# Kernel optimization log

Hardware: AMD Instinct MI355X
Metric: run time of the kernel (lower is better)

## Reference

```python
import jax, jax.numpy as jnp
import numpy as np

B, T, C, H, R = 2, 2048, 2048, 16, 8
D = C // H  # head_dim = 128


def _rope_cache(seq_len, dim, theta=10000.0):
    pos = jnp.arange(seq_len, dtype=jnp.float32)[:, None]            # [T,1]
    idx = jnp.arange(0, dim, 2, dtype=jnp.float32)                   # [D/2]
    freqs = 1.0 / (theta ** (idx / dim))
    ang = pos * freqs                                                # [T, D/2]
    return jnp.cos(ang), jnp.sin(ang)


def setup_inputs() -> dict:
    key = jax.random.key(0)
    ks = jax.random.split(key, 16)
    s = 0.02
    inp = {"x": jax.random.normal(ks[0], (B, T, C), dtype=jnp.float32)}
    i = 1
    for nm in ("q", "k", "v", "p"):
        inp[f"{nm}_w"] = jax.random.normal(ks[i], (C, C), dtype=jnp.float32) * s; i += 1
        inp[f"{nm}_b"] = jnp.zeros((C,), dtype=jnp.float32)
        inp[f"{nm}_A"] = jax.random.normal(ks[i], (C, R), dtype=jnp.float32) * s; i += 1
        inp[f"{nm}_B"] = jax.random.normal(ks[i], (R, C), dtype=jnp.float32) * s; i += 1
    cos, sin = _rope_cache(T, D)
    inp["cos"] = cos
    inp["sin"] = sin
    inp["mask"] = jnp.tril(jnp.ones((T, T), dtype=bool))  # causal SDPA mask
    inp["use_lora"] = 1
    return inp


def _lora_linear(x, w, b, A, Bm, use_lora):
    # base GEMM + bias, plus low-rank adapter x @ A @ B (intended path)
    out = x @ w.T + b
    if use_lora:
        out = out + (x @ A) @ Bm
    return out


def _apply_rope(x, cos, sin):
    # x: [B,H,T,D]; cos/sin: [T, D/2] broadcast over batch & heads
    x1 = x[..., ::2]
    x2 = x[..., 1::2]
    y = jnp.stack((x1 * cos - x2 * sin, x1 * sin + x2 * cos), axis=-1)
    return y.reshape(x.shape)


def reference(x, q_w, q_b, q_A, q_B, k_w, k_b, k_A, k_B,
              v_w, v_b, v_A, v_B, p_w, p_b, p_A, p_B,
              cos, sin, mask, use_lora):
    Bsz, Tl, Cd = x.shape
    q = _lora_linear(x, q_w, q_b, q_A, q_B, use_lora).reshape(Bsz, Tl, H, D).transpose(0, 2, 1, 3)
    k = _lora_linear(x, k_w, k_b, k_A, k_B, use_lora).reshape(Bsz, Tl, H, D).transpose(0, 2, 1, 3)
    v = _lora_linear(x, v_w, v_b, v_A, v_B, use_lora).reshape(Bsz, Tl, H, D).transpose(0, 2, 1, 3)
    q = _apply_rope(q, cos, sin)
    k = _apply_rope(k, cos, sin)
    # scaled dot-product attention with boolean mask (True = attend)
    scale = 1.0 / jnp.sqrt(jnp.asarray(D, dtype=x.dtype))
    scores = jnp.einsum('bhqd,bhkd->bhqk', q, k) * scale          # [B,H,T,T]
    neg = jnp.asarray(jnp.finfo(scores.dtype).min, dtype=scores.dtype)
    scores = jnp.where(mask, scores, neg)
    attn = jax.nn.softmax(scores, axis=-1)
    out = jnp.einsum('bhqk,bhkd->bhqd', attn, v)                  # [B,H,T,D]
    y = out.transpose(0, 2, 1, 3).reshape(Bsz, Tl, Cd)
    return _lora_linear(y, p_w, p_b, p_A, p_B, use_lora)
```

## Files before the change

### kernel.cpp

```cpp
#include <hip/hip_runtime.h>

typedef _Float16 f16;
typedef _Float16 f16x4 __attribute__((ext_vector_type(4)));
typedef _Float16 f16x8 __attribute__((ext_vector_type(8)));
typedef __fp16 hf2 __attribute__((ext_vector_type(2)));
typedef float f32x4 __attribute__((ext_vector_type(4)));

#define DEV static __device__ __forceinline__

DEV void gl_lds16(const void* g, void* l) {
  __builtin_amdgcn_global_load_lds(
      (const __attribute__((address_space(1))) void*)g,
      (__attribute__((address_space(3))) void*)l, 16, 0, 0);
}

DEV uint pkrtz(float a, float b) {
  hf2 h = __builtin_amdgcn_cvt_pkrtz(a, b);
  return __builtin_bit_cast(uint, h);
}

DEV f32x4 MFMA(f16x8 a, f16x8 b, f32x4 c) {
  return __builtin_amdgcn_mfma_f32_16x16x32_f16(a, b, c, 0, 0, 0);
}

#define SC2Q 0.12752551286084103f

__global__ void cast_w_kernel(const float* __restrict__ w0,
                              const float* __restrict__ w1,
                              const float* __restrict__ w2,
                              const float* __restrict__ w3,
                              f16* __restrict__ b0, f16* __restrict__ b1,
                              f16* __restrict__ b2, f16* __restrict__ b3) {
  const int total4 = 4 * 4194304 / 4;
  for (int i = blockIdx.x * blockDim.x + threadIdx.x; i < total4;
       i += gridDim.x * blockDim.x) {
    int e = i << 2;
    const float* s; f16* d; int off;
    if (e < 4194304)        { s = w0; d = b0; off = e; }
    else if (e < 8388608)   { s = w1; d = b1; off = e - 4194304; }
    else if (e < 12582912)  { s = w2; d = b2; off = e - 8388608; }
    else                    { s = w3; d = b3; off = e - 12582912; }
    float4 v = *(const float4*)(s + off);
    f16x4 hv = {(f16)v.x, (f16)v.y, (f16)v.z, (f16)v.w};
    *(f16x4*)(d + off) = hv;
  }
}

__global__ __launch_bounds__(256) void lora_x_kernel(
    const float* __restrict__ x, const float* __restrict__ Aq,
    const float* __restrict__ Ak, const float* __restrict__ Av,
    float* __restrict__ la, f16* __restrict__ xb) {
  const int wave = threadIdx.x >> 6, lane = threadIdx.x & 63;
  const int m = blockIdx.x * 4 + wave;
  const float* xrow = x + (size_t)m * 2048;
  f16* xbrow = xb + (size_t)m * 2048;
  const float* As[3] = {Aq, Ak, Av};
  float acc[3][8] = {};
  for (int i = 0; i < 32; ++i) {
    int k = i * 64 + lane;
    float xv = xrow[k];
    xbrow[k] = (f16)xv;
#pragma unroll
    for (int nm = 0; nm < 3; ++nm) {
      const float4* ap = (const float4*)(As[nm] + (size_t)k * 8);
      float4 a0 = ap[0], a1 = ap[1];
      acc[nm][0] += xv * a0.x; acc[nm][1] += xv * a0.y;
      acc[nm][2] += xv * a0.z; acc[nm][3] += xv * a0.w;
      acc[nm][4] += xv * a1.x; acc[nm][5] += xv * a1.y;
      acc[nm][6] += xv * a1.z; acc[nm][7] += xv * a1.w;
    }
  }
#pragma unroll
  for (int nm = 0; nm < 3; ++nm)
#pragma unroll
    for (int r = 0; r < 8; ++r) {
      float v = acc[nm][r];
#pragma unroll
      for (int off = 1; off < 64; off <<= 1) v += __shfl_xor(v, off);
      acc[nm][r] = v;
    }
  if (lane == 0) {
#pragma unroll
    for (int nm = 0; nm < 3; ++nm)
#pragma unroll
      for (int r = 0; r < 8; ++r)
        la[nm * 32768 + (size_t)m * 8 + r] = acc[nm][r];
  }
}

__global__ __launch_bounds__(256) void lora_p_kernel(
    const f16* __restrict__ y, const float* __restrict__ Ap,
    float* __restrict__ lap) {
  const int wave = threadIdx.x >> 6, lane = threadIdx.x & 63;
  const int m = blockIdx.x * 4 + wave;
  const f16* yrow = y + (size_t)m * 2048;
  float acc[8] = {};
  for (int i = 0; i < 4; ++i) {
    int k0 = i * 512 + lane * 8;
    f16x8 yv = *(const f16x8*)(yrow + k0);
#pragma unroll
    for (int j = 0; j < 8; ++j) {
      float xv = (float)yv[j];
      const float4* ap = (const float4*)(Ap + (size_t)(k0 + j) * 8);
      float4 a0 = ap[0], a1 = ap[1];
      acc[0] += xv * a0.x; acc[1] += xv * a0.y;
      acc[2] += xv * a0.z; acc[3] += xv * a0.w;
      acc[4] += xv * a1.x; acc[5] += xv * a1.y;
      acc[6] += xv * a1.z; acc[7] += xv * a1.w;
    }
  }
#pragma unroll
  for (int r = 0; r < 8; ++r) {
    float v = acc[r];
#pragma unroll
    for (int off = 1; off < 64; off <<= 1) v += __shfl_xor(v, off);
    acc[r] = v;
  }
  if (lane == 0) {
#pragma unroll
    for (int r = 0; r < 8; ++r) lap[(size_t)m * 8 + r] = acc[r];
  }
}

struct GemmArgs {
  const f16* A;
  const f16* W[3];
  const float* bias[3];
  const float* la[3];
  const float* Bm[3];
  void* out[3];
  int mode[3];
};

__global__ __launch_bounds__(256, 2) void gemm2_kernel(
    GemmArgs args, const int* __restrict__ use_lora,
    const float* __restrict__ cosT, const float* __restrict__ sinT) {
  extern __shared__ char smem[];
  const int z = blockIdx.y;
  const f16* A = args.A;
  const f16* Bw = args.W[z];
  const float* bias = args.bias[z];
  const float* la = args.la[z];
  const float* Bm = args.Bm[z];
  void* out = args.out[z];
  const int mode = args.mode[z];

  const int tid = threadIdx.x;
  const int wave = tid >> 6, lane = tid & 63;
  const int lr = lane & 15, lg = lane >> 4;
  const int bm = (int)blockIdx.x >> 4, bn = (int)blockIdx.x & 15;
  const int m0 = bm << 7, n0 = bn << 7;
  const int wr = wave >> 1, wc = wave & 1;

  const char* Ab = (const char*)A;
  const char* Bb = (const char*)Bw;

  uint aoff[4], boff[4];
#pragma unroll
  for (int r = 0; r < 4; ++r) {
    uint beta = (uint)(wave * 4 + r) * 1024 + (uint)lane * 16;
    uint row = beta >> 7;
    uint c = (beta & 127u) ^ ((row & 7u) << 4);
    aoff[r] = (uint)(m0 + row) * 4096 + c;
    boff[r] = (uint)(n0 + row) * 4096 + c;
  }

  auto STAGE = [&](int kt, int b) {
    char* dst = smem + b * 32768;
    const size_t kb = (size_t)kt << 7;
#pragma unroll
    for (int r = 0; r < 4; ++r) {
      gl_lds16(Ab + (aoff[r] + kb), dst + (wave * 4 + r) * 1024);
      gl_lds16(Bb + (boff[r] + kb), dst + 16384 + (wave * 4 + r) * 1024);
    }
  };

  f32x4 acc[4][4] = {};

  STAGE(0, 0);
  for (int kt = 0; kt < 32; ++kt) {
    const int b = kt & 1;
    asm volatile("s_waitcnt vmcnt(0) lgkmcnt(0)" ::: "memory");
    __builtin_amdgcn_s_barrier();
    if (kt + 1 < 32) STAGE(kt + 1, b ^ 1);

    const char* buf = smem + b * 32768;
    f16x8 af[2][4], bf[2][4];
#pragma unroll
    for (int ks = 0; ks < 2; ++ks) {
#pragma unroll
      for (int mi = 0; mi < 4; ++mi) {
        int row = wr * 64 + mi * 16 + lr;
        int c = (ks * 64 + lg * 16) ^ ((row & 7) << 4);
        af[ks][mi] = *(const f16x8*)(buf + row * 128 + c);
      }
#pragma unroll
      for (int ni = 0; ni < 4; ++ni) {
        int row = wc * 64 + ni * 16 + lr;
        int c = (ks * 64 + lg * 16) ^ ((row & 7) << 4);
        bf[ks][ni] = *(const f16x8*)(buf + 16384 + row * 128 + c);
      }
    }
    __builtin_amdgcn_s_setprio(1);
#pragma unroll
    for (int ks = 0; ks < 2; ++ks)
#pragma unroll
      for (int mi = 0; mi < 4; ++mi)
#pragma unroll
        for (int ni = 0; ni < 4; ++ni)
          acc[mi][ni] = MFMA(af[ks][mi], bf[ks][ni], acc[mi][ni]);
    __builtin_amdgcn_s_setprio(0);
  }

  const int ul = use_lora[0];
  asm volatile("s_waitcnt lgkmcnt(0)" ::: "memory");
  __builtin_amdgcn_s_barrier();

  float bv[4], bml[4][8];
#pragma unroll
  for (int ni = 0; ni < 4; ++ni) {
    int n = n0 + wc * 64 + ni * 16 + lr;
    bv[ni] = bias[n];
    if (ul) {
#pragma unroll
      for (int r = 0; r < 8; ++r) bml[ni][r] = Bm[r * 2048 + n];
    }
  }

#pragma unroll
  for (int mi = 0; mi < 4; ++mi) {
    const int mbase = m0 + wr * 64 + mi * 16 + lg * 4;
    float lar[4][8];
    if (ul) {
#pragma unroll
      for (int rg = 0; rg < 4; ++rg) {
        const float4* lp = (const float4*)(la + (size_t)(mbase + rg) * 8);
        float4 l0 = lp[0], l1 = lp[1];
        lar[rg][0] = l0.x; lar[rg][1] = l0.y; lar[rg][2] = l0.z; lar[rg][3] = l0.w;
        lar[rg][4] = l1.x; lar[rg][5] = l1.y; lar[rg][6] = l1.z; lar[rg][7] = l1.w;
      }
    }
#pragma unroll
    for (int ni = 0; ni < 4; ++ni) {
      const int n = n0 + wc * 64 + ni * 16 + lr;
#pragma unroll
      for (int rg = 0; rg < 4; ++rg) {
        float v = acc[mi][ni][rg] + bv[ni];
        if (ul) {
#pragma unroll
          for (int r = 0; r < 8; ++r) v += lar[rg][r] * bml[ni][r];
        }
        const int mm = wr * 64 + mi * 16 + lg * 4 + rg;
        const int nn = wc * 64 + ni * 16 + lr;
        if (mode <= 1) {
          float pv = __shfl_xor(v, 1);
          const int t = (mbase + rg) & 2047;
          const int ci = t * 64 + ((n & 127) >> 1);
          float cs = cosT[ci], sn = sinT[ci];
          float res = ((lane & 1) == 0) ? (v * cs - pv * sn)
                                        : (pv * sn + v * cs);
          if (mode == 0) res *= SC2Q;
          ((f16*)smem)[mm * 128 + nn] = (f16)res;
        } else if (mode == 2) {
          *(f16*)(smem + nn * 256 + ((mm * 2) ^ ((nn & 7) << 4))) = (f16)v;
        } else {
          ((float*)out)[(size_t)(mbase + rg) * 2048 + n] = v;
        }
      }
    }
  }

  if (mode <= 1) {
    __builtin_amdgcn_s_barrier();
    const long b_ = m0 >> 11;
    const int tb = m0 & 2047;
    char* obase = (char*)out + ((b_ * 16 + bn) * 2048 + tb) * 256;
#pragma unroll
    for (int p = 0; p < 8; ++p) {
      int s = p * 4096 + tid * 16;
      int row = s >> 8, c = s & 255;
      *(uint4*)(obase + (long)row * 256 + c) = *(const uint4*)(smem + s);
    }
  } else if (mode == 2) {
    __builtin_amdgcn_s_barrier();
    const long b_ = m0 >> 11;
    const int tb = m0 & 2047;
    char* obase = (char*)out + (((b_ * 16 + bn) * 128) * 2048 + tb) * 2;
#pragma unroll
    for (int p = 0; p < 8; ++p) {
      int s = p * 4096 + tid * 16;
      int row = s >> 8, cb = s & 255;
      int c = cb ^ ((row & 7) << 4);
      uint4 val = *(const uint4*)(smem + row * 256 + c);
      *(uint4*)(obase + (long)row * 4096 + cb) = val;
    }
  }
}

__global__ __launch_bounds__(256, 2) void attn_kernel(
    const f16* __restrict__ qr, const f16* __restrict__ kr,
    const f16* __restrict__ vt, f16* __restrict__ y) {
  extern __shared__ char smem[];
  const int tid = threadIdx.x, wave = tid >> 6, lane = tid & 63;
  const int lr = lane & 15, lg = lane >> 4;
  const int qt = 15 - (int)blockIdx.x;
  const int q0 = qt << 7;
  const int h = blockIdx.y, b = blockIdx.z;
  const long bh = b * 16 + h;
  const int nt = 2 * qt + 2;

  const char* kbase = (const char*)kr + bh * 2048 * 256;
  const char* vbase = (const char*)vt + bh * 128 * 4096;

  uint koff[4], voff[4];
#pragma unroll
  for (int r = 0; r < 4; ++r) {
    uint s = (uint)(wave * 4 + r) * 1024 + (uint)lane * 16;
    uint rowk = s >> 8;
    koff[r] = rowk * 256 + ((s & 255u) ^ ((rowk & 7u) << 4));
    uint rowv = s >> 7;
    voff[r] = rowv * 4096 + ((s & 127u) ^ ((rowv & 7u) << 4));
  }

  f16x8 qf[2][4];
#pragma unroll
  for (int g = 0; g < 2; ++g) {
    const char* qb =
        (const char*)qr + (bh * 2048 + q0 + wave * 32 + g * 16 + lr) * 256;
#pragma unroll
    for (int ks = 0; ks < 4; ++ks)
      qf[g][ks] = *(const f16x8*)(qb + ks * 64 + lg * 16);
  }

  f32x4 o[2][8] = {};
  float mrow[2] = {-3e38f, -3e38f};
  float lsum[2] = {0.f, 0.f};

  auto STAGE = [&](int kv0, int bsel) {
    char* Ks = smem + bsel * 32768;
    char* Vs = Ks + 16384;
#pragma unroll
    for (int r = 0; r < 4; ++r) {
      gl_lds16(kbase + (size_t)kv0 * 256 + koff[r], Ks + (wave * 4 + r) * 1024);
      gl_lds16(vbase + (size_t)kv0 * 2 + voff[r], Vs + (wave * 4 + r) * 1024);
    }
  };

  STAGE(0, 0);
  __syncthreads();

  for (int kt = 0; kt < nt; ++kt) {
    const int kv0 = kt << 6;
    if (kt + 1 < nt) STAGE((kt + 1) << 6, (kt + 1) & 1);
    const char* Ks = smem + (kt & 1) * 32768;
    const char* Vs = Ks + 16384;

    if (kv0 <= q0 + wave * 32 + 31) {
      f32x4 sa[2][4] = {};
      __builtin_amdgcn_s_setprio(1);
#pragma unroll
      for (int ks = 0; ks < 4; ++ks)
#pragma unroll
        for (int n = 0; n < 4; ++n) {
          int row = n * 16 + lr;
          int c = (ks * 64 + lg * 16) ^ ((row & 7) << 4);
          f16x8 kf = *(const f16x8*)(Ks + row * 256 + c);
          sa[0][n] = MFMA(kf, qf[0][ks], sa[0][n]);
          sa[1][n] = MFMA(kf, qf[1][ks], sa[1][n]);
        }
      __builtin_amdgcn_s_setprio(0);

      f16x8 pf[2][2];
#pragma unroll
      for (int g = 0; g < 2; ++g) {
        const int qgbase = q0 + wave * 32 + g * 16;
        float L[16];
        const bool dm = (kv0 + 63 > qgbase);
#pragma unroll
        for (int n = 0; n < 4; ++n)
#pragma unroll
          for (int rg = 0; rg < 4; ++rg) {
            float Lv = sa[g][n][rg];
            if (dm && (kv0 + n * 16 + lg * 4 + rg > qgbase + lr)) Lv = -3e37f;
            L[n * 4 + rg] = Lv;
          }
        float m0a = fmaxf(L[0], L[1]),  m1a = fmaxf(L[2], L[3]);
        float m2a = fmaxf(L[4], L[5]),  m3a = fmaxf(L[6], L[7]);
        float m4a = fmaxf(L[8], L[9]),  m5a = fmaxf(L[10], L[11]);
        float m6a = fmaxf(L[12], L[13]), m7a = fmaxf(L[14], L[15]);
        float m0b = fmaxf(m0a, m1a), m1b = fmaxf(m2a, m3a);
        float m2b = fmaxf(m4a, m5a), m3b = fmaxf(m6a, m7a);
        float pm = fmaxf(fmaxf(m0b, m1b), fmaxf(m2b, m3b));
        if (!__all(pm <= mrow[g] + 8.f)) {
          pm = fmaxf(pm, __shfl_xor(pm, 16));
          pm = fmaxf(pm, __shfl_xor(pm, 32));
          float mn = fmaxf(mrow[g], pm);
          float alpha = exp2f(mrow[g] - mn);
          mrow[g] = mn;
          lsum[g] *= alpha;
#pragma unroll
          for (int dt = 0; dt < 8; ++dt)
#pragma unroll
            for (int rg = 0; rg < 4; ++rg) o[g][dt][rg] *= alpha;
        }
        const float mn = mrow[g];
#pragma unroll
        for (int i = 0; i < 16; ++i) L[i] = exp2f(L[i] - mn);
        float s0 = L[0] + L[1], s1 = L[2] + L[3], s2 = L[4] + L[5],
              s3 = L[6] + L[7], s4 = L[8] + L[9], s5 = L[10] + L[11],
              s6 = L[12] + L[13], s7 = L[14] + L[15];
        float t0 = s0 + s1, t1 = s2 + s3, t2 = s4 + s5, t3 = s6 + s7;
        float ps = (t0 + t1) + (t2 + t3);
        ps += __shfl_xor(ps, 16);
        ps += __shfl_xor(ps, 32);
        lsum[g] += ps;

#pragma unroll
        for (int ks2 = 0; ks2 < 2; ++ks2) {
          uint w0 = pkrtz(L[8 * ks2 + 0], L[8 * ks2 + 1]);
          uint w1 = pkrtz(L[8 * ks2 + 2], L[8 * ks2 + 3]);
          uint w2 = pkrtz(L[8 * ks2 + 4], L[8 * ks2 + 5]);
          uint w3 = pkrtz(L[8 * ks2 + 6], L[8 * ks2 + 7]);
          int src1 = ((lg & 1) << 5) + lr;
          int src2 = src1 + 16;
          uint a0 = __shfl((int)w0, src1), a1 = __shfl((int)w1, src1);
          uint a2 = __shfl((int)w2, src1), a3 = __shfl((int)w3, src1);
          uint b0 = __shfl((int)w0, src2), b1 = __shfl((int)w1, src2);
          uint b2 = __shfl((int)w2, src2), b3 = __shfl((int)w3, src2);
          const bool hi = (lg >> 1) != 0;
          uint4 uu;
          uu.x = hi ? a2 : a0;
          uu.y = hi ? a3 : a1;
          uu.z = hi ? b2 : b0;
          uu.w = hi ? b3 : b1;
          pf[g][ks2] = __builtin_bit_cast(f16x8, uu);
        }
      }

#pragma unroll
      for (int ks2 = 0; ks2 < 2; ++ks2) {
        __builtin_amdgcn_s_setprio(1);
#pragma unroll
        for (int dt = 0; dt < 8; ++dt) {
          int drow = dt * 16 + lr;
          int c = (ks2 * 64 + lg * 16) ^ ((drow & 7) << 4);
          f16x8 vf = *(const f16x8*)(Vs + drow * 128 + c);
          o[0][dt] = MFMA(vf, pf[0][ks2], o[0][dt]);
          o[1][dt] = MFMA(vf, pf[1][ks2], o[1][dt]);
        }
        __builtin_amdgcn_s_setprio(0);
      }
    }
    __syncthreads();
  }

#pragma unroll
  for (int g = 0; g < 2; ++g) {
    const float inv = 1.f / lsum[g];
    const int row = wave * 32 + g * 16 + lr;
#pragma unroll
    for (int dt = 0; dt < 8; ++dt) {
      uint lo = pkrtz(o[g][dt][0] * inv, o[g][dt][1] * inv);
      uint hi2 = pkrtz(o[g][dt][2] * inv, o[g][dt][3] * inv);
      int c = (dt * 32 + lg * 8) ^ ((row & 7) << 4);
      uint2 w;
      w.x = lo;
      w.y = hi2;
      *(uint2*)(smem + row * 256 + c) = w;
    }
  }
  __syncthreads();
#pragma unroll
  for (int p = 0; p < 8; ++p) {
    int s = p * 4096 + tid * 16;
    int row = s >> 8, cb = s & 255;
    int c = cb ^ ((row & 7) << 4);
    char* dst =
        (char*)y + ((long)(b * 2048 + q0 + row) * 2048 + h * 128) * 2 + cb;
    *(uint4*)dst = *(const uint4*)(smem + row * 256 + c);
  }
}

extern "C" void kernel_launch(void* const* d_in, const int* in_sizes, int n_in,
                              void* d_out, int out_size, void* d_ws,
                              size_t ws_size, hipStream_t stream) {
  (void)in_sizes; (void)n_in; (void)out_size; (void)ws_size;
  const float* x   = (const float*)d_in[0];
  const float* q_w = (const float*)d_in[1];
  const float* q_b = (const float*)d_in[2];
  const float* q_A = (const float*)d_in[3];
  const float* q_B = (const float*)d_in[4];
  const float* k_w = (const float*)d_in[5];
  const float* k_b = (const float*)d_in[6];
  const float* k_A = (const float*)d_in[7];
  const float* k_B = (const float*)d_in[8];
  const float* v_w = (const float*)d_in[9];
  const float* v_b = (const float*)d_in[10];
  const float* v_A = (const float*)d_in[11];
  const float* v_B = (const float*)d_in[12];
  const float* p_w = (const float*)d_in[13];
  const float* p_b = (const float*)d_in[14];
  const float* p_A = (const float*)d_in[15];
  const float* p_B = (const float*)d_in[16];
  const float* cosT = (const float*)d_in[17];
  const float* sinT = (const float*)d_in[18];
  const int* use_lora = (const int*)d_in[20];

  char* ws = (char*)d_ws;
  f16* xb  = (f16*)(ws);
  f16* wqb = (f16*)(ws + 16777216);
  f16* wkb = (f16*)(ws + 25165824);
  f16* wvb = (f16*)(ws + 33554432);
  f16* wpb = (f16*)(ws + 41943040);
  float* la = (float*)(ws + 50331648);
  f16* qr  = (f16*)(ws + 50855936);
  f16* kr  = (f16*)(ws + 67633152);
  f16* vt  = (f16*)(ws + 84410368);
  f16* y   = xb;
  float* lap = la + 98304;

  cast_w_kernel<<<dim3(2048), dim3(256), 0, stream>>>(
      q_w, k_w, v_w, p_w, wqb, wkb, wvb, wpb);
  lora_x_kernel<<<dim3(1024), dim3(256), 0, stream>>>(x, q_A, k_A, v_A, la, xb);

  GemmArgs qkv;
  qkv.A = xb;
  qkv.W[0] = wqb;  qkv.W[1] = wkb;  qkv.W[2] = wvb;
  qkv.bias[0] = q_b; qkv.bias[1] = k_b; qkv.bias[2] = v_b;
  qkv.la[0] = la; qkv.la[1] = la + 32768; qkv.la[2] = la + 65536;
  qkv.Bm[0] = q_B; qkv.Bm[1] = k_B; qkv.Bm[2] = v_B;
  qkv.out[0] = qr; qkv.out[1] = kr; qkv.out[2] = vt;
  qkv.mode[0] = 0; qkv.mode[1] = 1; qkv.mode[2] = 2;
  gemm2_kernel<<<dim3(512, 3), dim3(256), 65536, stream>>>(
      qkv, use_lora, cosT, sinT);

  attn_kernel<<<dim3(16, 16, 2), dim3(256), 65536, stream>>>(qr, kr, vt, y);
  lora_p_kernel<<<dim3(1024), dim3(256), 0, stream>>>(y, p_A, lap);

  GemmArgs pp;
  pp.A = y;
  pp.W[0] = wpb;  pp.W[1] = wpb;  pp.W[2] = wpb;
  pp.bias[0] = p_b; pp.bias[1] = p_b; pp.bias[2] = p_b;
  pp.la[0] = lap; pp.la[1] = lap; pp.la[2] = lap;
  pp.Bm[0] = p_B; pp.Bm[1] = p_B; pp.Bm[2] = p_B;
  pp.out[0] = d_out; pp.out[1] = d_out; pp.out[2] = d_out;
  pp.mode[0] = 3; pp.mode[1] = 3; pp.mode[2] = 3;
  gemm2_kernel<<<dim3(512, 1), dim3(256), 65536, stream>>>(
      pp, use_lora, nullptr, nullptr);
}
```

Measured before the change: 369.6 us.

## Software-pipeline attention: overlap next tile's QK^T with current softmax and PV

```diff
diff --git a/kernel.cpp b/kernel.cpp
--- a/kernel.cpp
+++ b/kernel.cpp
@@ -308,6 +308,7 @@
   const int h = blockIdx.y, b = blockIdx.z;
   const long bh = b * 16 + h;
   const int nt = 2 * qt + 2;
+  const int wbound = q0 + wave * 32 + 31;
 
   const char* kbase = (const char*)kr + bh * 2048 * 256;
   const char* vbase = (const char*)vt + bh * 128 * 4096;
@@ -336,122 +337,141 @@
   float mrow[2] = {-3e38f, -3e38f};
   float lsum[2] = {0.f, 0.f};
 
-  auto STAGE = [&](int kv0, int bsel) {
-    char* Ks = smem + bsel * 32768;
-    char* Vs = Ks + 16384;
-#pragma unroll
-    for (int r = 0; r < 4; ++r) {
+  auto STAGE_K = [&](int kv0, int kbi) {
+    char* Ks = smem + kbi * 16384;
+#pragma unroll
+    for (int r = 0; r < 4; ++r)
       gl_lds16(kbase + (size_t)kv0 * 256 + koff[r], Ks + (wave * 4 + r) * 1024);
+  };
+  auto STAGE_V = [&](int kv0, int vbi) {
+    char* Vs = smem + 49152 + vbi * 16384;
+#pragma unroll
+    for (int r = 0; r < 4; ++r)
       gl_lds16(vbase + (size_t)kv0 * 2 + voff[r], Vs + (wave * 4 + r) * 1024);
-    }
   };
 
-  STAGE(0, 0);
+  auto QKT = [&](int kbi, f32x4 (&sa)[2][4]) {
+    const char* Ks = smem + kbi * 16384;
+#pragma unroll
+    for (int g = 0; g < 2; ++g)
+#pragma unroll
+      for (int n = 0; n < 4; ++n) sa[g][n] = f32x4{0.f, 0.f, 0.f, 0.f};
+    __builtin_amdgcn_s_setprio(1);
+#pragma unroll
+    for (int ks = 0; ks < 4; ++ks)
+#pragma unroll
+      for (int n = 0; n < 4; ++n) {
+        int row = n * 16 + lr;
+        int c = (ks * 64 + lg * 16) ^ ((row & 7) << 4);
+        f16x8 kf = *(const f16x8*)(Ks + row * 256 + c);
+        sa[0][n] = MFMA(kf, qf[0][ks], sa[0][n]);
+        sa[1][n] = MFMA(kf, qf[1][ks], sa[1][n]);
+      }
+    __builtin_amdgcn_s_setprio(0);
+  };
+
+  auto SOFTMAX_PV = [&](int kt, f32x4 (&sa)[2][4]) {
+    const int kv0 = kt << 6;
+    const char* Vs = smem + 49152 + (kt & 1) * 16384;
+    f16x8 pf[2][2];
+#pragma unroll
+    for (int g = 0; g < 2; ++g) {
+      const int qgbase = q0 + wave * 32 + g * 16;
+      float L[16];
+      const bool dm = (kv0 + 63 > qgbase);
+#pragma unroll
+      for (int n = 0; n < 4; ++n)
+#pragma unroll
+        for (int rg = 0; rg < 4; ++rg) {
+          float Lv = sa[g][n][rg];
+          if (dm && (kv0 + n * 16 + lg * 4 + rg > qgbase + lr)) Lv = -3e37f;
+          L[n * 4 + rg] = Lv;
+        }
+      float m0a = fmaxf(L[0], L[1]),  m1a = fmaxf(L[2], L[3]);
+      float m2a = fmaxf(L[4], L[5]),  m3a = fmaxf(L[6], L[7]);
+      float m4a = fmaxf(L[8], L[9]),  m5a = fmaxf(L[10], L[11]);
+      float m6a = fmaxf(L[12], L[13]), m7a = fmaxf(L[14], L[15]);
+      float m0b = fmaxf(m0a, m1a), m1b = fmaxf(m2a, m3a);
+      float m2b = fmaxf(m4a, m5a), m3b = fmaxf(m6a, m7a);
+      float pm = fmaxf(fmaxf(m0b, m1b), fmaxf(m2b, m3b));
+      if (!__all(pm <= mrow[g] + 8.f)) {
+        pm = fmaxf(pm, __shfl_xor(pm, 16));
+        pm = fmaxf(pm, __shfl_xor(pm, 32));
+        float mn = fmaxf(mrow[g], pm);
+        float alpha = exp2f(mrow[g] - mn);
+        mrow[g] = mn;
+        lsum[g] *= alpha;
+#pragma unroll
+        for (int dt = 0; dt < 8; ++dt)
+#pragma unroll
+          for (int rg = 0; rg < 4; ++rg) o[g][dt][rg] *= alpha;
+      }
+      const float mn = mrow[g];
+#pragma unroll
+      for (int i = 0; i < 16; ++i) L[i] = exp2f(L[i] - mn);
+      float s0 = L[0] + L[1], s1 = L[2] + L[3], s2 = L[4] + L[5],
+            s3 = L[6] + L[7], s4 = L[8] + L[9], s5 = L[10] + L[11],
+            s6 = L[12] + L[13], s7 = L[14] + L[15];
+      float t0 = s0 + s1, t1 = s2 + s3, t2 = s4 + s5, t3 = s6 + s7;
+      float ps = (t0 + t1) + (t2 + t3);
+      ps += __shfl_xor(ps, 16);
+      ps += __shfl_xor(ps, 32);
+      lsum[g] += ps;
+
+#pragma unroll
+      for (int ks2 = 0; ks2 < 2; ++ks2) {
+        uint w0 = pkrtz(L[8 * ks2 + 0], L[8 * ks2 + 1]);
+        uint w1 = pkrtz(L[8 * ks2 + 2], L[8 * ks2 + 3]);
+        uint w2 = pkrtz(L[8 * ks2 + 4], L[8 * ks2 + 5]);
+        uint w3 = pkrtz(L[8 * ks2 + 6], L[8 * ks2 + 7]);
+        int src1 = ((lg & 1) << 5) + lr;
+        int src2 = src1 + 16;
+        uint a0 = __shfl((int)w0, src1), a1 = __shfl((int)w1, src1);
+        uint a2 = __shfl((int)w2, src1), a3 = __shfl((int)w3, src1);
+        uint b0 = __shfl((int)w0, src2), b1 = __shfl((int)w1, src2);
+        uint b2 = __shfl((int)w2, src2), b3 = __shfl((int)w3, src2);
+        const bool hi = (lg >> 1) != 0;
+        uint4 uu;
+        uu.x = hi ? a2 : a0;
+        uu.y = hi ? a3 : a1;
+        uu.z = hi ? b2 : b0;
+        uu.w = hi ? b3 : b1;
+        pf[g][ks2] = __builtin_bit_cast(f16x8, uu);
+      }
+    }
+#pragma unroll
+    for (int ks2 = 0; ks2 < 2; ++ks2) {
+      __builtin_amdgcn_s_setprio(1);
+#pragma unroll
+      for (int dt = 0; dt < 8; ++dt) {
+        int drow = dt * 16 + lr;
+        int c = (ks2 * 64 + lg * 16) ^ ((drow & 7) << 4);
+        f16x8 vf = *(const f16x8*)(Vs + drow * 128 + c);
+        o[0][dt] = MFMA(vf, pf[0][ks2], o[0][dt]);
+        o[1][dt] = MFMA(vf, pf[1][ks2], o[1][dt]);
+      }
+      __builtin_amdgcn_s_setprio(0);
+    }
+  };
+
+  auto ITER = [&](int kt, f32x4 (&cur)[2][4], f32x4 (&nxt)[2][4]) {
+    if (kt + 1 < nt) STAGE_V((kt + 1) << 6, (kt + 1) & 1);
+    if (kt + 2 < nt) STAGE_K((kt + 2) << 6, (kt + 2) % 3);
+    if (kt + 1 < nt && ((kt + 1) << 6) <= wbound) QKT((kt + 1) % 3, nxt);
+    if ((kt << 6) <= wbound) SOFTMAX_PV(kt, cur);
+    __syncthreads();
+  };
+
+  STAGE_K(0, 0);
+  STAGE_V(0, 0);
+  STAGE_K(64, 1);
   __syncthreads();
-
-  for (int kt = 0; kt < nt; ++kt) {
-    const int kv0 = kt << 6;
-    if (kt + 1 < nt) STAGE((kt + 1) << 6, (kt + 1) & 1);
-    const char* Ks = smem + (kt & 1) * 32768;
-    const char* Vs = Ks + 16384;
-
-    if (kv0 <= q0 + wave * 32 + 31) {
-      f32x4 sa[2][4] = {};
-      __builtin_amdgcn_s_setprio(1);
-#pragma unroll
-      for (int ks = 0; ks < 4; ++ks)
-#pragma unroll
-        for (int n = 0; n < 4; ++n) {
-          int row = n * 16 + lr;
-          int c = (ks * 64 + lg * 16) ^ ((row & 7) << 4);
-          f16x8 kf = *(const f16x8*)(Ks + row * 256 + c);
-          sa[0][n] = MFMA(kf, qf[0][ks], sa[0][n]);
-          sa[1][n] = MFMA(kf, qf[1][ks], sa[1][n]);
-        }
-      __builtin_amdgcn_s_setprio(0);
-
-      f16x8 pf[2][2];
-#pragma unroll
-      for (int g = 0; g < 2; ++g) {
-        const int qgbase = q0 + wave * 32 + g * 16;
-        float L[16];
-        const bool dm = (kv0 + 63 > qgbase);
-#pragma unroll
-        for (int n = 0; n < 4; ++n)
-#pragma unroll
-          for (int rg = 0; rg < 4; ++rg) {
-            float Lv = sa[g][n][rg];
-            if (dm && (kv0 + n * 16 + lg * 4 + rg > qgbase + lr)) Lv = -3e37f;
-            L[n * 4 + rg] = Lv;
-          }
-        float m0a = fmaxf(L[0], L[1]),  m1a = fmaxf(L[2], L[3]);
-        float m2a = fmaxf(L[4], L[5]),  m3a = fmaxf(L[6], L[7]);
-        float m4a = fmaxf(L[8], L[9]),  m5a = fmaxf(L[10], L[11]);
-        float m6a = fmaxf(L[12], L[13]), m7a = fmaxf(L[14], L[15]);
-        float m0b = fmaxf(m0a, m1a), m1b = fmaxf(m2a, m3a);
-        float m2b = fmaxf(m4a, m5a), m3b = fmaxf(m6a, m7a);
-        float pm = fmaxf(fmaxf(m0b, m1b), fmaxf(m2b, m3b));
-        if (!__all(pm <= mrow[g] + 8.f)) {
-          pm = fmaxf(pm, __shfl_xor(pm, 16));
-          pm = fmaxf(pm, __shfl_xor(pm, 32));
-          float mn = fmaxf(mrow[g], pm);
-          float alpha = exp2f(mrow[g] - mn);
-          mrow[g] = mn;
-          lsum[g] *= alpha;
-#pragma unroll
-          for (int dt = 0; dt < 8; ++dt)
-#pragma unroll
-            for (int rg = 0; rg < 4; ++rg) o[g][dt][rg] *= alpha;
-        }
-        const float mn = mrow[g];
-#pragma unroll
-        for (int i = 0; i < 16; ++i) L[i] = exp2f(L[i] - mn);
-        float s0 = L[0] + L[1], s1 = L[2] + L[3], s2 = L[4] + L[5],
-              s3 = L[6] + L[7], s4 = L[8] + L[9], s5 = L[10] + L[11],
-              s6 = L[12] + L[13], s7 = L[14] + L[15];
-        float t0 = s0 + s1, t1 = s2 + s3, t2 = s4 + s5, t3 = s6 + s7;
-        float ps = (t0 + t1) + (t2 + t3);
-        ps += __shfl_xor(ps, 16);
-        ps += __shfl_xor(ps, 32);
-        lsum[g] += ps;
-
-#pragma unroll
-        for (int ks2 = 0; ks2 < 2; ++ks2) {
-          uint w0 = pkrtz(L[8 * ks2 + 0], L[8 * ks2 + 1]);
-          uint w1 = pkrtz(L[8 * ks2 + 2], L[8 * ks2 + 3]);
-          uint w2 = pkrtz(L[8 * ks2 + 4], L[8 * ks2 + 5]);
-          uint w3 = pkrtz(L[8 * ks2 + 6], L[8 * ks2 + 7]);
-          int src1 = ((lg & 1) << 5) + lr;
-          int src2 = src1 + 16;
-          uint a0 = __shfl((int)w0, src1), a1 = __shfl((int)w1, src1);
-          uint a2 = __shfl((int)w2, src1), a3 = __shfl((int)w3, src1);
-          uint b0 = __shfl((int)w0, src2), b1 = __shfl((int)w1, src2);
-          uint b2 = __shfl((int)w2, src2), b3 = __shfl((int)w3, src2);
-          const bool hi = (lg >> 1) != 0;
-          uint4 uu;
-          uu.x = hi ? a2 : a0;
-          uu.y = hi ? a3 : a1;
-          uu.z = hi ? b2 : b0;
-          uu.w = hi ? b3 : b1;
-          pf[g][ks2] = __builtin_bit_cast(f16x8, uu);
-        }
-      }
-
-#pragma unroll
-      for (int ks2 = 0; ks2 < 2; ++ks2) {
-        __builtin_amdgcn_s_setprio(1);
-#pragma unroll
-        for (int dt = 0; dt < 8; ++dt) {
-          int drow = dt * 16 + lr;
-          int c = (ks2 * 64 + lg * 16) ^ ((drow & 7) << 4);
-          f16x8 vf = *(const f16x8*)(Vs + drow * 128 + c);
-          o[0][dt] = MFMA(vf, pf[0][ks2], o[0][dt]);
-          o[1][dt] = MFMA(vf, pf[1][ks2], o[1][dt]);
-        }
-        __builtin_amdgcn_s_setprio(0);
-      }
-    }
-    __syncthreads();
+  f32x4 saA[2][4], saB[2][4];
+  QKT(0, saA);
+
+  for (int t = 0; t < nt; t += 2) {
+    ITER(t, saA, saB);
+    ITER(t + 1, saB, saA);
   }
 
 #pragma unroll
@@ -534,7 +554,7 @@
   gemm2_kernel<<<dim3(512, 3), dim3(256), 65536, stream>>>(
       qkv, use_lora, cosT, sinT);
 
-  attn_kernel<<<dim3(16, 16, 2), dim3(256), 65536, stream>>>(qr, kr, vt, y);
+  attn_kernel<<<dim3(16, 16, 2), dim3(256), 81920, stream>>>(qr, kr, vt, y);
   lora_p_kernel<<<dim3(1024), dim3(256), 0, stream>>>(y, p_A, lap);
 
   GemmArgs pp;
```

Measured after the change: 374.7 us. No clear change (+1.4%).

## Fold LoRA adapters into fp16 weights during cast and drop separate LoRA kernels

Applied to the files above, without the earlier changes.

```diff
diff --git a/kernel.cpp b/kernel.cpp
--- a/kernel.cpp
+++ b/kernel.cpp
@@ -25,100 +25,60 @@
 
 #define SC2Q 0.12752551286084103f
 
-__global__ void cast_w_kernel(const float* __restrict__ w0,
-                              const float* __restrict__ w1,
-                              const float* __restrict__ w2,
-                              const float* __restrict__ w3,
-                              f16* __restrict__ b0, f16* __restrict__ b1,
-                              f16* __restrict__ b2, f16* __restrict__ b3) {
-  const int total4 = 4 * 4194304 / 4;
-  for (int i = blockIdx.x * blockDim.x + threadIdx.x; i < total4;
-       i += gridDim.x * blockDim.x) {
-    int e = i << 2;
-    const float* s; f16* d; int off;
-    if (e < 4194304)        { s = w0; d = b0; off = e; }
-    else if (e < 8388608)   { s = w1; d = b1; off = e - 4194304; }
-    else if (e < 12582912)  { s = w2; d = b2; off = e - 8388608; }
-    else                    { s = w3; d = b3; off = e - 12582912; }
-    float4 v = *(const float4*)(s + off);
-    f16x4 hv = {(f16)v.x, (f16)v.y, (f16)v.z, (f16)v.w};
-    *(f16x4*)(d + off) = hv;
-  }
-}
-
-__global__ __launch_bounds__(256) void lora_x_kernel(
-    const float* __restrict__ x, const float* __restrict__ Aq,
-    const float* __restrict__ Ak, const float* __restrict__ Av,
-    float* __restrict__ la, f16* __restrict__ xb) {
-  const int wave = threadIdx.x >> 6, lane = threadIdx.x & 63;
-  const int m = blockIdx.x * 4 + wave;
-  const float* xrow = x + (size_t)m * 2048;
-  f16* xbrow = xb + (size_t)m * 2048;
-  const float* As[3] = {Aq, Ak, Av};
-  float acc[3][8] = {};
-  for (int i = 0; i < 32; ++i) {
-    int k = i * 64 + lane;
-    float xv = xrow[k];
-    xbrow[k] = (f16)xv;
-#pragma unroll
-    for (int nm = 0; nm < 3; ++nm) {
-      const float4* ap = (const float4*)(As[nm] + (size_t)k * 8);
-      float4 a0 = ap[0], a1 = ap[1];
-      acc[nm][0] += xv * a0.x; acc[nm][1] += xv * a0.y;
-      acc[nm][2] += xv * a0.z; acc[nm][3] += xv * a0.w;
-      acc[nm][4] += xv * a1.x; acc[nm][5] += xv * a1.y;
-      acc[nm][6] += xv * a1.z; acc[nm][7] += xv * a1.w;
-    }
-  }
-#pragma unroll
-  for (int nm = 0; nm < 3; ++nm)
-#pragma unroll
-    for (int r = 0; r < 8; ++r) {
-      float v = acc[nm][r];
-#pragma unroll
-      for (int off = 1; off < 64; off <<= 1) v += __shfl_xor(v, off);
-      acc[nm][r] = v;
-    }
-  if (lane == 0) {
-#pragma unroll
-    for (int nm = 0; nm < 3; ++nm)
-#pragma unroll
-      for (int r = 0; r < 8; ++r)
-        la[nm * 32768 + (size_t)m * 8 + r] = acc[nm][r];
-  }
-}
-
-__global__ __launch_bounds__(256) void lora_p_kernel(
-    const f16* __restrict__ y, const float* __restrict__ Ap,
-    float* __restrict__ lap) {
-  const int wave = threadIdx.x >> 6, lane = threadIdx.x & 63;
-  const int m = blockIdx.x * 4 + wave;
-  const f16* yrow = y + (size_t)m * 2048;
-  float acc[8] = {};
-  for (int i = 0; i < 4; ++i) {
-    int k0 = i * 512 + lane * 8;
-    f16x8 yv = *(const f16x8*)(yrow + k0);
-#pragma unroll
-    for (int j = 0; j < 8; ++j) {
-      float xv = (float)yv[j];
-      const float4* ap = (const float4*)(Ap + (size_t)(k0 + j) * 8);
-      float4 a0 = ap[0], a1 = ap[1];
-      acc[0] += xv * a0.x; acc[1] += xv * a0.y;
-      acc[2] += xv * a0.z; acc[3] += xv * a0.w;
-      acc[4] += xv * a1.x; acc[5] += xv * a1.y;
-      acc[6] += xv * a1.z; acc[7] += xv * a1.w;
-    }
-  }
-#pragma unroll
-  for (int r = 0; r < 8; ++r) {
-    float v = acc[r];
-#pragma unroll
-    for (int off = 1; off < 64; off <<= 1) v += __shfl_xor(v, off);
-    acc[r] = v;
-  }
-  if (lane == 0) {
-#pragma unroll
-    for (int r = 0; r < 8; ++r) lap[(size_t)m * 8 + r] = acc[r];
+__global__ __launch_bounds__(256) void prep_kernel(
+    const float* __restrict__ x, f16* __restrict__ xb,
+    const float* __restrict__ w0, const float* __restrict__ A0,
+    const float* __restrict__ B0, f16* __restrict__ o0,
+    const float* __restrict__ w1, const float* __restrict__ A1,
+    const float* __restrict__ B1, f16* __restrict__ o1,
+    const float* __restrict__ w2, const float* __restrict__ A2,
+    const float* __restrict__ B2, f16* __restrict__ o2,
+    const float* __restrict__ w3, const float* __restrict__ A3,
+    const float* __restrict__ B3, f16* __restrict__ o3,
+    const int* __restrict__ use_lora) {
+  const float ul = (float)use_lora[0];
+  const int gid = blockIdx.x * 256 + threadIdx.x;
+  const int stride = gridDim.x * 256;
+  const int XF4 = 2097152;
+  const int WF4 = 1048576;
+
+  for (int i = gid; i < XF4; i += stride) {
+    float4 v = ((const float4*)x)[i];
+    f16x4 h = {(f16)v.x, (f16)v.y, (f16)v.z, (f16)v.w};
+    ((f16x4*)xb)[i] = h;
+  }
+
+  const float* Ws[4] = {w0, w1, w2, w3};
+  const float* As[4] = {A0, A1, A2, A3};
+  const float* Bs[4] = {B0, B1, B2, B3};
+  f16* Os[4] = {o0, o1, o2, o3};
+#pragma unroll
+  for (int wsel = 0; wsel < 4; ++wsel) {
+    const float* W = Ws[wsel];
+    const float* A = As[wsel];
+    const float* Bm = Bs[wsel];
+    f16* O = Os[wsel];
+    for (int i = gid; i < WF4; i += stride) {
+      const int n = i >> 9;
+      const int k = (i & 511) << 2;
+      float4 wv = ((const float4*)W)[i];
+      float bcol[8];
+#pragma unroll
+      for (int r = 0; r < 8; ++r) bcol[r] = Bm[r * 2048 + n];
+      const float4* Ap = (const float4*)(A + (size_t)k * 8);
+      float ov[4];
+      const float* wp = &wv.x;
+#pragma unroll
+      for (int j = 0; j < 4; ++j) {
+        float4 a0 = Ap[j * 2], a1 = Ap[j * 2 + 1];
+        float s = a0.x * bcol[0] + a0.y * bcol[1] + a0.z * bcol[2] +
+                  a0.w * bcol[3] + a1.x * bcol[4] + a1.y * bcol[5] +
+                  a1.z * bcol[6] + a1.w * bcol[7];
+        ov[j] = wp[j] + ul * s;
+      }
+      f16x4 h = {(f16)ov[0], (f16)ov[1], (f16)ov[2], (f16)ov[3]};
+      ((f16x4*)O)[i] = h;
+    }
   }
 }
 
@@ -126,22 +86,18 @@
   const f16* A;
   const f16* W[3];
   const float* bias[3];
-  const float* la[3];
-  const float* Bm[3];
   void* out[3];
   int mode[3];
 };
 
 __global__ __launch_bounds__(256, 2) void gemm2_kernel(
-    GemmArgs args, const int* __restrict__ use_lora,
-    const float* __restrict__ cosT, const float* __restrict__ sinT) {
+    GemmArgs args, const float* __restrict__ cosT,
+    const float* __restrict__ sinT) {
   extern __shared__ char smem[];
   const int z = blockIdx.y;
   const f16* A = args.A;
   const f16* Bw = args.W[z];
   const float* bias = args.bias[z];
-  const float* la = args.la[z];
-  const float* Bm = args.Bm[z];
   void* out = args.out[z];
   const int mode = args.mode[z];
 
@@ -212,44 +168,22 @@
     __builtin_amdgcn_s_setprio(0);
   }
 
-  const int ul = use_lora[0];
   asm volatile("s_waitcnt lgkmcnt(0)" ::: "memory");
   __builtin_amdgcn_s_barrier();
 
-  float bv[4], bml[4][8];
-#pragma unroll
-  for (int ni = 0; ni < 4; ++ni) {
-    int n = n0 + wc * 64 + ni * 16 + lr;
-    bv[ni] = bias[n];
-    if (ul) {
-#pragma unroll
-      for (int r = 0; r < 8; ++r) bml[ni][r] = Bm[r * 2048 + n];
-    }
-  }
+  float bv[4];
+#pragma unroll
+  for (int ni = 0; ni < 4; ++ni) bv[ni] = bias[n0 + wc * 64 + ni * 16 + lr];
 
 #pragma unroll
   for (int mi = 0; mi < 4; ++mi) {
     const int mbase = m0 + wr * 64 + mi * 16 + lg * 4;
-    float lar[4][8];
-    if (ul) {
-#pragma unroll
-      for (int rg = 0; rg < 4; ++rg) {
-        const float4* lp = (const float4*)(la + (size_t)(mbase + rg) * 8);
-        float4 l0 = lp[0], l1 = lp[1];
-        lar[rg][0] = l0.x; lar[rg][1] = l0.y; lar[rg][2] = l0.z; lar[rg][3] = l0.w;
-        lar[rg][4] = l1.x; lar[rg][5] = l1.y; lar[rg][6] = l1.z; lar[rg][7] = l1.w;
-      }
-    }
 #pragma unroll
     for (int ni = 0; ni < 4; ++ni) {
       const int n = n0 + wc * 64 + ni * 16 + lr;
 #pragma unroll
       for (int rg = 0; rg < 4; ++rg) {
         float v = acc[mi][ni][rg] + bv[ni];
-        if (ul) {
-#pragma unroll
-          for (int r = 0; r < 8; ++r) v += lar[rg][r] * bml[ni][r];
-        }
         const int mm = wr * 64 + mi * 16 + lg * 4 + rg;
         const int nn = wc * 64 + ni * 16 + lr;
         if (mode <= 1) {
@@ -512,39 +446,31 @@
   f16* wkb = (f16*)(ws + 25165824);
   f16* wvb = (f16*)(ws + 33554432);
   f16* wpb = (f16*)(ws + 41943040);
-  float* la = (float*)(ws + 50331648);
   f16* qr  = (f16*)(ws + 50855936);
   f16* kr  = (f16*)(ws + 67633152);
   f16* vt  = (f16*)(ws + 84410368);
   f16* y   = xb;
-  float* lap = la + 98304;
-
-  cast_w_kernel<<<dim3(2048), dim3(256), 0, stream>>>(
-      q_w, k_w, v_w, p_w, wqb, wkb, wvb, wpb);
-  lora_x_kernel<<<dim3(1024), dim3(256), 0, stream>>>(x, q_A, k_A, v_A, la, xb);
+
+  prep_kernel<<<dim3(2048), dim3(256), 0, stream>>>(
+      x, xb, q_w, q_A, q_B, wqb, k_w, k_A, k_B, wkb, v_w, v_A, v_B, wvb, p_w,
+      p_A, p_B, wpb, use_lora);
 
   GemmArgs qkv;
   qkv.A = xb;
   qkv.W[0] = wqb;  qkv.W[1] = wkb;  qkv.W[2] = wvb;
   qkv.bias[0] = q_b; qkv.bias[1] = k_b; qkv.bias[2] = v_b;
-  qkv.la[0] = la; qkv.la[1] = la + 32768; qkv.la[2] = la + 65536;
-  qkv.Bm[0] = q_B; qkv.Bm[1] = k_B; qkv.Bm[2] = v_B;
   qkv.out[0] = qr; qkv.out[1] = kr; qkv.out[2] = vt;
   qkv.mode[0] = 0; qkv.mode[1] = 1; qkv.mode[2] = 2;
-  gemm2_kernel<<<dim3(512, 3), dim3(256), 65536, stream>>>(
-      qkv, use_lora, cosT, sinT);
+  gemm2_kernel<<<dim3(512, 3), dim3(256), 65536, stream>>>(qkv, cosT, sinT);
 
   attn_kernel<<<dim3(16, 16, 2), dim3(256), 65536, stream>>>(qr, kr, vt, y);
-  lora_p_kernel<<<dim3(1024), dim3(256), 0, stream>>>(y, p_A, lap);
 
   GemmArgs pp;
   pp.A = y;
   pp.W[0] = wpb;  pp.W[1] = wpb;  pp.W[2] = wpb;
   pp.bias[0] = p_b; pp.bias[1] = p_b; pp.bias[2] = p_b;
-  pp.la[0] = lap; pp.la[1] = lap; pp.la[2] = lap;
-  pp.Bm[0] = p_B; pp.Bm[1] = p_B; pp.Bm[2] = p_B;
   pp.out[0] = d_out; pp.out[1] = d_out; pp.out[2] = d_out;
   pp.mode[0] = 3; pp.mode[1] = 3; pp.mode[2] = 3;
-  gemm2_kernel<<<dim3(512, 1), dim3(256), 65536, stream>>>(
-      pp, use_lora, nullptr, nullptr);
-}
+  gemm2_kernel<<<dim3(512, 1), dim3(256), 65536, stream>>>(pp, nullptr,
+                                                           nullptr);
+}
```

Result: faster. 345.1 us, median of 3 (-6.6%).
